# Optimization experiments

Measured on AMD Instinct MI355X. Metric: run time of the kernel, lower is better.

## Reference

```python
import jax, jax.numpy as jnp
import numpy as np

NUM_JOINTS = 50
FEAT = 3 * NUM_JOINTS  # 150

def _skeleton_bones():
    # Standard 50-joint sign-language skeleton (body + two 21-joint hands).
    body = [(0, 1), (1, 2), (2, 3), (3, 4), (1, 5), (5, 6), (6, 7)]
    def hand(conn_from, wrist):
        bones = [(conn_from, wrist)]
        for f in range(5):  # 5 fingers, chains of 4 joints from the wrist
            base = wrist + 1 + 4 * f
            bones.append((wrist, base))
            for k in range(3):
                bones.append((base + k, base + k + 1))
        return bones
    bones = body + hand(7, 8) + hand(4, 29)  # 49 bones
    bones.append((0, 2))  # pad to 50 bones so 3*num_bones == 150 matches the mask
    return np.asarray(bones, dtype=np.int32)

_BONES = _skeleton_bones()
_BA = jnp.asarray(_BONES[:, 0])  # (50,) bone endpoint a
_BB = jnp.asarray(_BONES[:, 1])  # (50,) bone endpoint b

def get_length_direct(x):
    # x: (B, T, 150) -> lengths (B, T, 50), directs (B, T, 150)
    B, T, _ = x.shape
    joints = x.reshape(B, T, NUM_JOINTS, 3)
    diff = joints[:, :, _BA, :] - joints[:, :, _BB, :]  # (B, T, 50, 3)
    length = jnp.sqrt(jnp.sum(diff * diff, axis=-1, keepdims=True))  # (B, T, 50, 1)
    tiny = jnp.finfo(x.dtype).tiny
    direct = diff / (length + tiny)  # unit directions
    return length[..., 0], direct.reshape(B, T, -1)

def setup_inputs() -> dict:
    key = jax.random.key(0)
    k1, k2 = jax.random.split(key)
    B, T = 64, 4096
    preds = jax.random.normal(k1, (B, T, FEAT), dtype=jnp.float32)
    targets = jax.random.normal(k2, (B, T, FEAT), dtype=jnp.float32)
    return {"preds": preds, "targets": targets}

def reference(preds, targets):
    target_pad = 0.0
    m = (targets != target_pad).astype(preds.dtype)  # (B, T, 150)
    pm = preds * m
    tm = targets * m
    _, pd = get_length_direct(pm)   # (B, T, 150)
    _, td = get_length_direct(tm)
    pd = pd * m  # mask[:, :, :150] == full mask since 3*num_bones == 150
    td = td * m
    # criterion = L1 (mean), criterion_bone = MSE (mean)
    recon = jnp.mean(jnp.abs(pm - tm)) + 0.1 * jnp.mean((pd - td) ** 2)
    return recon
```

## Files before the change

kernel.cpp:

```cpp
#include <hip/hip_runtime.h>

#define NUM_BONES  50
#define FEAT       150
#define FRAMES_PER_BLOCK 32
#define THREADS    256
#define TILE_ELEMS (FRAMES_PER_BLOCK * FEAT)
#define N4         (TILE_ELEMS / 4)
#define NLOAD      5
#define TINY_F     1.17549435e-38f
#define TOTAL_TILES      ((64 * 4096) / FRAMES_PER_BLOCK)
#define GRID_BLOCKS      1024
#define TILES_PER_BLOCK  (TOTAL_TILES / GRID_BLOCKS)

__device__ __constant__ int c_ba[NUM_BONES] = {
    0, 1, 2, 3, 1, 5, 6,
    7, 8, 9, 10, 11, 8, 13, 14, 15, 8, 17, 18, 19,
    8, 21, 22, 23, 8, 25, 26, 27,
    4, 29, 30, 31, 32, 29, 34, 35, 36, 29, 38, 39, 40,
    29, 42, 43, 44, 29, 46, 47, 48,
    0
};
__device__ __constant__ int c_bb[NUM_BONES] = {
    1, 2, 3, 4, 5, 6, 7,
    8, 9, 10, 11, 12, 13, 14, 15, 16, 17, 18, 19, 20,
    21, 22, 23, 24, 25, 26, 27, 28,
    29, 30, 31, 32, 33, 34, 35, 36, 37, 38, 39, 40, 41,
    42, 43, 44, 45, 46, 47, 48, 49,
    2
};

__global__ __launch_bounds__(THREADS)
void loss_main(const float* __restrict__ preds,
               const float* __restrict__ targets,
               double* __restrict__ part0,
               double* __restrict__ part1)
{
    __shared__ float s_pm[TILE_ELEMS];
    __shared__ float s_tm[TILE_ELEMS];

    const int tid = threadIdx.x;
    float l1  = 0.0f;
    float mse = 0.0f;

    for (int j = 0; j < TILES_PER_BLOCK; ++j) {
        const int tile = blockIdx.x + j * GRID_BLOCKS;
        const long long base = (long long)tile * TILE_ELEMS;
        const float4* p4 = (const float4*)(preds + base);
        const float4* t4 = (const float4*)(targets + base);
        float4* spm4 = (float4*)s_pm;
        float4* stm4 = (float4*)s_tm;

        float4 pr[NLOAD], tr[NLOAD];
#pragma unroll
        for (int k = 0; k < NLOAD; ++k) {
            int i = tid + k * THREADS;
            int ic = (i < N4) ? i : (N4 - 1);
            pr[k] = p4[ic];
            tr[k] = t4[ic];
        }

#pragma unroll
        for (int k = 0; k < NLOAD; ++k) {
            int i = tid + k * THREADS;
            if (i < N4) {
                float4 p = pr[k];
                float4 t = tr[k];
                float4 pm;
                pm.x = (t.x != 0.0f) ? p.x : 0.0f;
                pm.y = (t.y != 0.0f) ? p.y : 0.0f;
                pm.z = (t.z != 0.0f) ? p.z : 0.0f;
                pm.w = (t.w != 0.0f) ? p.w : 0.0f;
                l1 += fabsf(pm.x - t.x) + fabsf(pm.y - t.y)
                    + fabsf(pm.z - t.z) + fabsf(pm.w - t.w);
                spm4[i] = pm;
                stm4[i] = t;
            }
        }
        __syncthreads();

        const int ntask = FRAMES_PER_BLOCK * NUM_BONES;
#pragma unroll
        for (int k = 0; k < 7; ++k) {
            const int i = tid + k * THREADS;
            if (i < ntask) {
                const int f = i & 31;
                const int b = i >> 5;
                const float* pm = s_pm + f * FEAT;
                const float* tm = s_tm + f * FEAT;
                const int ja = 3 * c_ba[b];
                const int jb = 3 * c_bb[b];

                float dpx = pm[ja]     - pm[jb];
                float dpy = pm[ja + 1] - pm[jb + 1];
                float dpz = pm[ja + 2] - pm[jb + 2];
                float dtx = tm[ja]     - tm[jb];
                float dty = tm[ja + 1] - tm[jb + 1];
                float dtz = tm[ja + 2] - tm[jb + 2];

                float lp = sqrtf(dpx * dpx + dpy * dpy + dpz * dpz);
                float lt = sqrtf(dtx * dtx + dty * dty + dtz * dtz);
                float ip = 1.0f / (lp + TINY_F);
                float it = 1.0f / (lt + TINY_F);

                const int o = 3 * b;
                float e0 = dpx * ip - dtx * it;
                float e1 = dpy * ip - dty * it;
                float e2 = dpz * ip - dtz * it;
                if (tm[o]     != 0.0f) mse += e0 * e0;
                if (tm[o + 1] != 0.0f) mse += e1 * e1;
                if (tm[o + 2] != 0.0f) mse += e2 * e2;
            }
        }
        __syncthreads();
    }

    double v0 = (double)l1;
    double v1 = (double)mse;
    for (int off = 32; off > 0; off >>= 1) {
        v0 += __shfl_down(v0, off, 64);
        v1 += __shfl_down(v1, off, 64);
    }
    __shared__ double s_red0[THREADS / 64];
    __shared__ double s_red1[THREADS / 64];
    const int wave = tid >> 6;
    const int lane = tid & 63;
    if (lane == 0) { s_red0[wave] = v0; s_red1[wave] = v1; }
    __syncthreads();
    if (tid == 0) {
        part0[blockIdx.x] = s_red0[0] + s_red0[1] + s_red0[2] + s_red0[3];
        part1[blockIdx.x] = s_red1[0] + s_red1[1] + s_red1[2] + s_red1[3];
    }
}

__global__ __launch_bounds__(THREADS)
void loss_final(const double* __restrict__ part0,
                const double* __restrict__ part1,
                float* __restrict__ out)
{
    const int tid = threadIdx.x;
    double a = 0.0, b = 0.0;
    for (int i = tid; i < GRID_BLOCKS; i += THREADS) {
        a += part0[i];
        b += part1[i];
    }
    for (int off = 32; off > 0; off >>= 1) {
        a += __shfl_down(a, off, 64);
        b += __shfl_down(b, off, 64);
    }
    __shared__ double s0[THREADS / 64];
    __shared__ double s1[THREADS / 64];
    const int wave = tid >> 6;
    const int lane = tid & 63;
    if (lane == 0) { s0[wave] = a; s1[wave] = b; }
    __syncthreads();
    if (tid == 0) {
        double sa = s0[0] + s0[1] + s0[2] + s0[3];
        double sb = s1[0] + s1[1] + s1[2] + s1[3];
        const double N = 64.0 * 4096.0 * 150.0;
        out[0] = (float)(sa / N + 0.1 * (sb / N));
    }
}

extern "C" void kernel_launch(void* const* d_in, const int* in_sizes, int n_in,
                              void* d_out, int out_size, void* d_ws, size_t ws_size,
                              hipStream_t stream)
{
    (void)in_sizes; (void)n_in; (void)out_size; (void)ws_size;
    const float* preds   = (const float*)d_in[0];
    const float* targets = (const float*)d_in[1];
    double* part0 = (double*)d_ws;
    double* part1 = part0 + GRID_BLOCKS;

    loss_main<<<GRID_BLOCKS, THREADS, 0, stream>>>(preds, targets, part0, part1);
    loss_final<<<1, THREADS, 0, stream>>>(part0, part1, (float*)d_out);
}
```

Before: 324.9 us.

## Prefetch next tile into registers during bone compute and use rsq

Loads for the next tile are issued into registers right after the shared-memory tile is written, so global memory latency overlaps the bone-direction compute of the current tile. The per-bone sqrt plus divide is replaced with a single hardware reciprocal square root guarded against zero. The masked accumulation is also made branchless. The trade-offs are higher register pressure from holding the prefetched values and slightly different rounding from the approximate rsq.

```diff
diff --git a/kernel.cpp b/kernel.cpp
--- a/kernel.cpp
+++ b/kernel.cpp
@@ -7,7 +7,6 @@
 #define TILE_ELEMS (FRAMES_PER_BLOCK * FEAT)
 #define N4         (TILE_ELEMS / 4)
 #define NLOAD      5
-#define TINY_F     1.17549435e-38f
 #define TOTAL_TILES      ((64 * 4096) / FRAMES_PER_BLOCK)
 #define GRID_BLOCKS      1024
 #define TILES_PER_BLOCK  (TOTAL_TILES / GRID_BLOCKS)
@@ -42,23 +41,30 @@
     float l1  = 0.0f;
     float mse = 0.0f;
 
-    for (int j = 0; j < TILES_PER_BLOCK; ++j) {
-        const int tile = blockIdx.x + j * GRID_BLOCKS;
-        const long long base = (long long)tile * TILE_ELEMS;
-        const float4* p4 = (const float4*)(preds + base);
-        const float4* t4 = (const float4*)(targets + base);
-        float4* spm4 = (float4*)s_pm;
-        float4* stm4 = (float4*)s_tm;
+    const float4* pbase = (const float4*)preds;
+    const float4* tbase = (const float4*)targets;
+    float4* spm4 = (float4*)s_pm;
+    float4* stm4 = (float4*)s_tm;
 
-        float4 pr[NLOAD], tr[NLOAD];
+    int idx[NLOAD];
+#pragma unroll
+    for (int k = 0; k < NLOAD; ++k) {
+        int i = tid + k * THREADS;
+        idx[k] = (i < N4) ? i : (N4 - 1);
+    }
+
+    float4 pr[NLOAD], tr[NLOAD];
+    {
+        const long long t0 = (long long)blockIdx.x * N4;
 #pragma unroll
         for (int k = 0; k < NLOAD; ++k) {
-            int i = tid + k * THREADS;
-            int ic = (i < N4) ? i : (N4 - 1);
-            pr[k] = p4[ic];
-            tr[k] = t4[ic];
+            pr[k] = pbase[t0 + idx[k]];
+            tr[k] = tbase[t0 + idx[k]];
         }
+    }
 
+#pragma unroll 1
+    for (int j = 0; j < TILES_PER_BLOCK; ++j) {
 #pragma unroll
         for (int k = 0; k < NLOAD; ++k) {
             int i = tid + k * THREADS;
@@ -77,6 +83,16 @@
             }
         }
         __syncthreads();
+
+        if (j + 1 < TILES_PER_BLOCK) {
+            const long long tn =
+                (long long)(blockIdx.x + (j + 1) * GRID_BLOCKS) * N4;
+#pragma unroll
+            for (int k = 0; k < NLOAD; ++k) {
+                pr[k] = pbase[tn + idx[k]];
+                tr[k] = tbase[tn + idx[k]];
+            }
+        }
 
         const int ntask = FRAMES_PER_BLOCK * NUM_BONES;
 #pragma unroll
@@ -97,18 +113,18 @@
                 float dty = tm[ja + 1] - tm[jb + 1];
                 float dtz = tm[ja + 2] - tm[jb + 2];
 
-                float lp = sqrtf(dpx * dpx + dpy * dpy + dpz * dpz);
-                float lt = sqrtf(dtx * dtx + dty * dty + dtz * dtz);
-                float ip = 1.0f / (lp + TINY_F);
-                float it = 1.0f / (lt + TINY_F);
+                float lp2 = dpx * dpx + dpy * dpy + dpz * dpz;
+                float lt2 = dtx * dtx + dty * dty + dtz * dtz;
+                float ip = (lp2 > 0.0f) ? __builtin_amdgcn_rsqf(lp2) : 0.0f;
+                float it = (lt2 > 0.0f) ? __builtin_amdgcn_rsqf(lt2) : 0.0f;
 
                 const int o = 3 * b;
                 float e0 = dpx * ip - dtx * it;
                 float e1 = dpy * ip - dty * it;
                 float e2 = dpz * ip - dtz * it;
-                if (tm[o]     != 0.0f) mse += e0 * e0;
-                if (tm[o + 1] != 0.0f) mse += e1 * e1;
-                if (tm[o + 2] != 0.0f) mse += e2 * e2;
+                mse += (tm[o]     != 0.0f) ? e0 * e0 : 0.0f;
+                mse += (tm[o + 1] != 0.0f) ? e1 * e1 : 0.0f;
+                mse += (tm[o + 2] != 0.0f) ? e2 * e2 : 0.0f;
             }
         }
         __syncthreads();
```

Measured after the change: 323.9 us. No clear change (-0.3%).
